# Performance work log

Hardware: AMD Instinct MI355X
Metric: run time of the kernel (lower is better)

The kernel has to match this reference:

```python
import math
import jax, jax.numpy as jnp
import numpy as np

D = 768      # hidden_size
H = 16       # num_attention_heads (hardcoded in module)
DH = D // H  # value dim per head
SEQ = 512    # fpos/tpos are taken modulo 512
EPS = 1e-5   # torch LayerNorm default
SCALE = math.sqrt(D / H)  # attention_head_size = dim_key_query_all / num_heads


def _collab_attn(h, fpos, tpos, Wq, Wk, Wcb, Wv, bv, mix, Wd, bd, lng, lnb):
    """CollaborativeAttention.forward on one segment. h: [SEQ, D]."""
    fpos = fpos % SEQ
    tpos = tpos % SEQ
    fs = h[fpos]                                   # [F, D] gathered 'from' nodes
    ts = h[tpos]                                   # [T, D] gathered 'to' nodes
    q = fs @ Wq.T                                  # [F, D] (no bias)
    k = ts @ Wk.T                                  # [T, D] (no bias)
    mq = q[None, :, :] * mix[:, None, :]           # [H, F, D] per-head mixing
    scores = jnp.einsum('hfd,td->hft', mq, k)      # [H, F, T] full-D contraction
    cb = (ts @ Wcb.T).T                            # [H, T] content bias
    scores = (scores + cb[:, None, :]) / SCALE
    probs = jax.nn.softmax(scores, axis=-1)        # dropout = identity at eval
    v = (ts @ Wv.T + bv).reshape(-1, H, DH).transpose(1, 0, 2)  # [H, T, DH]
    ctx = jnp.einsum('hft,htd->hfd', probs, v)     # [H, F, DH]
    ctx = ctx.transpose(1, 0, 2).reshape(-1, D) @ Wd.T + bd      # [F, D]
    x = fs + ctx                                   # residual on gathered nodes
    mu = x.mean(-1, keepdims=True)
    var = ((x - mu) ** 2).mean(-1, keepdims=True)
    return lng * (x - mu) / jnp.sqrt(var + EPS) + lnb


def _encoder(hidden_states, fpos, tpos, qtoc, ctoq):
    outs = []
    for b in range(3):  # fixed small segment count, matches original unrolling
        o1 = _collab_attn(hidden_states[b], fpos[b], tpos[b], *qtoc).mean(0)
        o2 = _collab_attn(hidden_states[b], tpos[b], fpos[b], *ctoq).mean(0)
        outs.append(jnp.concatenate([o1, o2]))
    return jnp.stack(outs)  # [3, 2*D]


def setup_inputs() -> dict:
    key = jax.random.key(0)
    ks = jax.random.split(key, 32)
    inp = {
        'hidden_states': jax.random.normal(ks[0], (3, SEQ, D), jnp.float32),
        'fpos': jax.random.randint(ks[1], (3, 2048), 0, SEQ, jnp.int32),
        'tpos': jax.random.randint(ks[2], (3, 2048), 0, SEQ, jnp.int32),
    }
    i = 3
    for p in ('qtoc', 'ctoq'):
        for n, shape, std in (('Wq', (D, D), 0.02), ('Wk', (D, D), 0.02),
                              ('Wcb', (H, D), 0.02), ('Wv', (D, D), 0.02),
                              ('Wd', (D, D), 0.02), ('mix', (H, D), 0.2)):
            inp[p + '_' + n] = std * jax.random.normal(ks[i], shape, jnp.float32)
            i += 1
        inp[p + '_bv'] = jnp.zeros((D,), jnp.float32)
        inp[p + '_bd'] = jnp.zeros((D,), jnp.float32)
        inp[p + '_lng'] = jnp.ones((D,), jnp.float32)
        inp[p + '_lnb'] = jnp.zeros((D,), jnp.float32)
    return inp


def reference(hidden_states, fpos, tpos,
              qtoc_Wq, qtoc_Wk, qtoc_Wcb, qtoc_Wv, qtoc_Wd, qtoc_mix,
              qtoc_bv, qtoc_bd, qtoc_lng, qtoc_lnb,
              ctoq_Wq, ctoq_Wk, ctoq_Wcb, ctoq_Wv, ctoq_Wd, ctoq_mix,
              ctoq_bv, ctoq_bd, ctoq_lng, ctoq_lnb):
    qtoc = (qtoc_Wq, qtoc_Wk, qtoc_Wcb, qtoc_Wv, qtoc_bv, qtoc_mix,
            qtoc_Wd, qtoc_bd, qtoc_lng, qtoc_lnb)
    ctoq = (ctoq_Wq, ctoq_Wk, ctoq_Wcb, ctoq_Wv, ctoq_bv, ctoq_mix,
            ctoq_Wd, ctoq_bd, ctoq_lng, ctoq_lnb)
    return _encoder(hidden_states, fpos, tpos, qtoc, ctoq)
```

## Files before the change

kernel.cpp:

```cpp
#include <hip/hip_runtime.h>
#include <math.h>

#define DD 768
#define HH 16
#define DHH 48
#define NPOS 512
#define NIDX 2048
#define INV_SCALE 0.14433756729740643f
#define LN_EPS 1e-5f

typedef __bf16 bf16_t;
typedef __bf16 bf16x8 __attribute__((ext_vector_type(8)));
typedef float f32x4 __attribute__((ext_vector_type(4)));

__device__ __forceinline__ void g2lds16(const void* g, void* l) {
  __builtin_amdgcn_global_load_lds((const __attribute__((address_space(1))) void*)g,
                                   (__attribute__((address_space(3))) void*)l, 16, 0, 0);
}
__device__ __forceinline__ int stg_chunk(int lane) { return (lane & 3) ^ ((lane >> 3) & 3); }
__device__ __forceinline__ int rd_off(int row, int lq) {
  return row * 32 + ((lq ^ ((row >> 1) & 3)) << 3);
}

struct CvtDesc { const float* src; bf16_t* dst; int n8; };
struct CvtBatch { CvtDesc d[13]; };

__global__ __launch_bounds__(256) void prep(const int* __restrict__ fpos,
                                            const int* __restrict__ tpos,
                                            int* __restrict__ CNT, CvtBatch cvb) {
  const int bid = blockIdx.x;
  const int tid = threadIdx.x;
  __shared__ int shist[NPOS];
  if (bid < 6) {
    const int b = bid >> 1, which = bid & 1;
    const int* src = (which ? tpos : fpos) + b * NIDX;
    for (int i = tid; i < NPOS; i += 256) shist[i] = 0;
    __syncthreads();
    for (int i = tid; i < NIDX; i += 256) atomicAdd(&shist[src[i] & (NPOS - 1)], 1);
    __syncthreads();
    for (int i = tid; i < NPOS; i += 256) CNT[bid * NPOS + i] = shist[i];
    return;
  }
  const CvtDesc de = cvb.d[(bid - 6) >> 6];
  for (int i = ((bid - 6) & 63) * 256 + tid; i < de.n8; i += 64 * 256) {
    bf16_t t[8];
    if (de.src) {
      const f32x4 a = *(const f32x4*)(de.src + (size_t)i * 8);
      const f32x4 b = *(const f32x4*)(de.src + (size_t)i * 8 + 4);
#pragma unroll
      for (int e = 0; e < 4; ++e) { t[e] = (bf16_t)a[e]; t[4 + e] = (bf16_t)b[e]; }
    } else {
#pragma unroll
      for (int e = 0; e < 8; ++e) t[e] = (bf16_t)0.f;
    }
    *(bf16x8*)(de.dst + (size_t)i * 8) = *(bf16x8*)t;
  }
}

struct MDesc { const bf16_t* A; const bf16_t* B; const float* bias; void* C;
               float* cb; int mode; int ntiles; };
struct MBatch { MDesc d[18]; };

__global__ __launch_bounds__(256, 4) void gemm64(MBatch batch) {
  const MDesc de = batch.d[blockIdx.y];
  const int mt = blockIdx.x & 7, nt = blockIdx.x >> 3;
  if (nt >= de.ntiles) return;
  const int m0 = mt * 64, n0 = nt * 128;

  __shared__ bf16_t SA[2][2048];
  __shared__ bf16_t SB[2][4096];

  const int tid = threadIdx.x;
  const int w = tid >> 6, lane = tid & 63;
  const int wm = w >> 1, wn = w & 1;
  const int lm = lane & 15, lq = lane >> 4;
  const int sr = lane >> 2, sc = stg_chunk(lane);

  f32x4 acc[2][4] = {};

  auto stage = [&](int buf, int k0) {
#pragma unroll
    for (int c = 0; c < 3; ++c) {
      const int issue = w + c * 4;
      if (issue < 4)
        g2lds16(de.A + (size_t)(m0 + issue * 16 + sr) * 768 + k0 + sc * 8,
                SA[buf] + issue * 512);
      else {
        const int e = issue - 4;
        g2lds16(de.B + (size_t)(n0 + e * 16 + sr) * 768 + k0 + sc * 8,
                SB[buf] + e * 512);
      }
    }
  };

  stage(0, 0);
  for (int k0i = 0; k0i < 24; ++k0i) {
    const int cur = k0i & 1;
    __syncthreads();
    if (k0i + 1 < 24) stage(cur ^ 1, (k0i + 1) * 32);
    bf16x8 af[2], bfr[4];
#pragma unroll
    for (int i = 0; i < 2; ++i)
      af[i] = *(const bf16x8*)(SA[cur] + rd_off(wm * 32 + i * 16 + lm, lq));
#pragma unroll
    for (int j = 0; j < 4; ++j)
      bfr[j] = *(const bf16x8*)(SB[cur] + rd_off(wn * 64 + j * 16 + lm, lq));
#pragma unroll
    for (int i = 0; i < 2; ++i)
#pragma unroll
      for (int j = 0; j < 4; ++j)
        acc[i][j] = __builtin_amdgcn_mfma_f32_16x16x32_bf16(af[i], bfr[j], acc[i][j], 0, 0, 0);
  }

#pragma unroll
  for (int i = 0; i < 2; ++i) {
    const int rbase = m0 + wm * 32 + i * 16 + lq * 4;
#pragma unroll
    for (int j = 0; j < 4; ++j) {
      const int c = n0 + wn * 64 + j * 16 + lm;
      const float bv = (de.bias && c < 768) ? de.bias[c] : 0.f;
#pragma unroll
      for (int r = 0; r < 4; ++r) {
        const float v = acc[i][j][r] + bv;
        if (de.mode == 0)      ((float*)de.C)[(size_t)(rbase + r) * 768 + c] = v;
        else if (de.mode == 1) ((bf16_t*)de.C)[(size_t)(rbase + r) * 768 + c] = (bf16_t)v;
        else if (de.mode == 2) ((bf16_t*)de.C)[(size_t)c * NPOS + rbase + r] = (bf16_t)v;
        else {
          if (c < 768)       ((bf16_t*)de.C)[(size_t)(rbase + r) * 768 + c] = (bf16_t)v;
          else if (c < 784)  de.cb[(size_t)(rbase + r) * 16 + (c - 768)] = v;
        }
      }
    }
  }
}

__global__ __launch_bounds__(512, 4) void attn_mfma(
    const bf16_t* __restrict__ Qg, const bf16_t* __restrict__ Kg,
    const bf16_t* __restrict__ Vt, const float* __restrict__ cbG,
    const int* __restrict__ CNT, const float* __restrict__ mix0,
    const float* __restrict__ mix1, bf16_t* __restrict__ CTX) {
  const int bid = blockIdx.x;
  const int pd = bid >> 7;
  const int hg = (bid >> 4) & 7;
  const int ft = bid & 15;
  const int dir = pd & 1;
  const int f0 = ft * 32;

  __shared__ bf16_t U[17408];
  __shared__ bf16_t Vs[64 * 264];
  __shared__ float mixs[2][768];
  __shared__ float cbw[2][512];
  __shared__ float rowl[2][32];

  const int tid = threadIdx.x;
  const int w = tid >> 6, lane = tid & 63;
  const int hh = w & 1, jq = w >> 1;
  const int lm = lane & 15, lq = lane >> 4;
  const int sr = lane >> 2, sc = stg_chunk(lane);

  const bf16_t* Qp = Qg + (size_t)pd * NPOS * DD;
  const bf16_t* Kp = Kg + (size_t)pd * NPOS * DD;
  const float* mixsel = dir ? mix1 : mix0;
  const int* cnt = CNT + ((pd & ~1) + (1 - dir)) * NPOS;

  for (int i = tid; i < 2 * 768; i += 512) {
    const int h2 = i / 768, c = i % 768;
    mixs[h2][c] = mixsel[(hg * 2 + h2) * DD + c] * INV_SCALE;
  }
  for (int i = tid; i < 2 * 512; i += 512) {
    const int h2 = i >> 9, j = i & 511;
    cbw[h2][j] = cbG[((size_t)pd * NPOS + j) * HH + hg * 2 + h2] * INV_SCALE
               + __logf((float)cnt[j]);
  }
  for (int i = tid; i < 16 * 264; i += 512) {
    const int r = 48 + i / 264, c = i % 264;
    Vs[r * 264 + c] = (bf16_t)((r == 48 && c < 256) ? 1.f : 0.f);
  }

  f32x4 sa[2][8] = {};

  for (int k0i = 0; k0i < 24; ++k0i) {
    const int k0 = k0i * 32;
    __syncthreads();
#pragma unroll
    for (int c = 0; c < 5; ++c) {
      const int issue = w + c * 8;
      if (issue < 2)
        g2lds16(Qp + (size_t)(f0 + issue * 16 + sr) * DD + k0 + sc * 8,
                U + issue * 512);
      else if (issue < 34) {
        const int e = issue - 2;
        g2lds16(Kp + (size_t)(e * 16 + sr) * DD + k0 + sc * 8,
                U + 1024 + e * 512);
      }
    }
    __syncthreads();

    const f32x4 mxa = *(const f32x4*)&mixs[hh][k0 + lq * 8];
    const f32x4 mxb = *(const f32x4*)&mixs[hh][k0 + lq * 8 + 4];
    bf16x8 af[2];
#pragma unroll
    for (int i = 0; i < 2; ++i) {
      const bf16x8 q = *(const bf16x8*)(U + rd_off(i * 16 + lm, lq));
      bf16_t t[8];
#pragma unroll
      for (int e = 0; e < 4; ++e) {
        t[e]     = (bf16_t)((float)q[e] * mxa[e]);
        t[4 + e] = (bf16_t)((float)q[4 + e] * mxb[e]);
      }
      af[i] = *(bf16x8*)t;
    }
#pragma unroll
    for (int jj = 0; jj < 8; ++jj) {
      const bf16x8 bf = *(const bf16x8*)(U + 1024 + rd_off(jq * 128 + jj * 16 + lm, lq));
      sa[0][jj] = __builtin_amdgcn_mfma_f32_16x16x32_bf16(af[0], bf, sa[0][jj], 0, 0, 0);
      sa[1][jj] = __builtin_amdgcn_mfma_f32_16x16x32_bf16(af[1], bf, sa[1][jj], 0, 0, 0);
    }
  }
  __syncthreads();

  const int fi = w & 1, cj = w >> 1;
  f32x4 pv[2] = {};

  for (int ph = 0; ph < 2; ++ph) {
    const int h = hg * 2 + ph;
    const bf16_t* Vp = Vt + (size_t)pd * DD * NPOS + (size_t)h * DHH * NPOS;

    if (hh == ph) {
#pragma unroll
      for (int jj = 0; jj < 8; ++jj) {
        const int col = jq * 128 + jj * 16 + lm;
        const float cb = cbw[ph][col];
#pragma unroll
        for (int i = 0; i < 2; ++i) {
          const int rb = i * 16 + lq * 4;
#pragma unroll
          for (int r = 0; r < 4; ++r)
            U[(rb + r) * 532 + col] = (bf16_t)__expf(sa[i][jj][r] + cb);
        }
      }
    }

    for (int vh = 0; vh < 2; ++vh) {
      for (int i = tid; i < 48 * 32; i += 512) {
        const int r = i >> 5, cc = i & 31;
        *(bf16x8*)(Vs + r * 264 + cc * 8) =
            *(const bf16x8*)(Vp + (size_t)r * NPOS + vh * 256 + cc * 8);
      }
      __syncthreads();
#pragma unroll
      for (int kk = 0; kk < 8; ++kk) {
        const bf16x8 pa = *(const bf16x8*)(U + (fi * 16 + lm) * 532 + vh * 256 + kk * 32 + lq * 8);
        const bf16x8 pb = *(const bf16x8*)(Vs + (cj * 16 + lm) * 264 + kk * 32 + lq * 8);
        pv[ph] = __builtin_amdgcn_mfma_f32_16x16x32_bf16(pa, pb, pv[ph], 0, 0, 0);
      }
      __syncthreads();
    }
    if (cj == 3 && lm == 0) {
#pragma unroll
      for (int r = 0; r < 4; ++r) rowl[ph][fi * 16 + lq * 4 + r] = pv[ph][r];
    }
  }
  __syncthreads();

  if (cj < 3) {
#pragma unroll
    for (int ph = 0; ph < 2; ++ph) {
      const int h = hg * 2 + ph;
#pragma unroll
      for (int r = 0; r < 4; ++r) {
        const int fr = fi * 16 + lq * 4 + r;
        CTX[((size_t)pd * NPOS + f0 + fr) * DD + h * DHH + cj * 16 + lm] =
            (bf16_t)(pv[ph][r] / rowl[ph][fr]);
      }
    }
  }
}

__global__ __launch_bounds__(256) void ln_mean_kernel(
    const float* __restrict__ hs, const float* __restrict__ XB,
    const int* __restrict__ CNT,
    const float* __restrict__ lng0, const float* __restrict__ lnb0,
    const float* __restrict__ lng1, const float* __restrict__ lnb1,
    float* __restrict__ out) {
  const int blk = blockIdx.x;
  const int chunk = blk & 63;
  const int pd = blk >> 6;
  const int b = pd >> 1, dir = pd & 1;
  const float* lng = dir ? lng1 : lng0;
  const float* lnb = dir ? lnb1 : lnb0;
  const int* cnt = CNT + pd * NPOS;
  const float* hb = hs + (size_t)b * NPOS * DD;
  const float* xb = XB + (size_t)pd * NPOS * DD;

  __shared__ float wacc[4][DD];
  const int tid = threadIdx.x;
  const int wave = tid >> 6, lane = tid & 63;
  for (int d0 = tid; d0 < 4 * DD; d0 += 256) ((float*)wacc)[d0] = 0.f;
  __syncthreads();

  float lg[12], lb[12];
#pragma unroll
  for (int qd = 0; qd < 12; ++qd) {
    lg[qd] = lng[lane + qd * 64];
    lb[qd] = lnb[lane + qd * 64];
  }

  for (int rr = 0; rr < 2; ++rr) {
    const int p = chunk * 8 + wave * 2 + rr;
    float x[12];
    float s = 0.f, ss = 0.f;
#pragma unroll
    for (int qd = 0; qd < 12; ++qd) {
      const int d0 = lane + qd * 64;
      const float xv = hb[(size_t)p * DD + d0] + xb[(size_t)p * DD + d0];
      x[qd] = xv; s += xv; ss += xv * xv;
    }
#pragma unroll
    for (int o = 1; o < 64; o <<= 1) {
      s += __shfl_xor(s, o);
      ss += __shfl_xor(ss, o);
    }
    const float mu = s * (1.f / 768.f);
    const float var = ss * (1.f / 768.f) - mu * mu;
    const float rstd = rsqrtf(var + LN_EPS);
    const float wgt = (float)cnt[p];
    if (wgt != 0.f) {
#pragma unroll
      for (int qd = 0; qd < 12; ++qd) {
        const int d0 = lane + qd * 64;
        wacc[wave][d0] += wgt * (lg[qd] * (x[qd] - mu) * rstd + lb[qd]);
      }
    }
  }
  __syncthreads();
  for (int d0 = tid; d0 < DD; d0 += 256) {
    const float t = wacc[0][d0] + wacc[1][d0] + wacc[2][d0] + wacc[3][d0];
    atomicAdd(&out[b * 1536 + dir * 768 + d0], t * (1.f / 2048.f));
  }
}

extern "C" void kernel_launch(void* const* d_in, const int* in_sizes, int n_in,
                              void* d_out, int out_size, void* d_ws, size_t ws_size,
                              hipStream_t stream) {
  const float* hs  = (const float*)d_in[0];
  const int* fpos  = (const int*)d_in[1];
  const int* tpos  = (const int*)d_in[2];

  const float* Wq[2]; const float* Wk[2]; const float* Wcb[2]; const float* Wv[2];
  const float* Wd[2]; const float* mixp[2];
  const float* bv[2]; const float* bd[2]; const float* lng[2]; const float* lnb[2];
  for (int p = 0; p < 2; ++p) {
    const int base = 3 + p * 10;
    Wq[p]   = (const float*)d_in[base + 0];
    Wk[p]   = (const float*)d_in[base + 1];
    Wcb[p]  = (const float*)d_in[base + 2];
    Wv[p]   = (const float*)d_in[base + 3];
    Wd[p]   = (const float*)d_in[base + 4];
    mixp[p] = (const float*)d_in[base + 5];
    bv[p]   = (const float*)d_in[base + 6];
    bd[p]   = (const float*)d_in[base + 7];
    lng[p]  = (const float*)d_in[base + 8];
    lnb[p]  = (const float*)d_in[base + 9];
  }

  char* wsp = (char*)d_ws;
  size_t off = 0;
  auto alloc = [&](size_t bytes) { char* p = wsp + off; off = (off + bytes + 255) & ~(size_t)255; return p; };
  bf16_t* hsb  = (bf16_t*)alloc((size_t)3 * NPOS * DD * 2);
  bf16_t* Wb   = (bf16_t*)alloc((size_t)6 * DD * DD * 2);
  bf16_t* WkCb = (bf16_t*)alloc((size_t)2 * 896 * DD * 2);
  bf16_t* Qbf  = (bf16_t*)alloc((size_t)6 * NPOS * DD * 2);
  bf16_t* Kbf  = (bf16_t*)alloc((size_t)6 * NPOS * DD * 2);
  bf16_t* VtG  = (bf16_t*)alloc((size_t)6 * DD * NPOS * 2);
  bf16_t* CTXb = (bf16_t*)alloc((size_t)6 * NPOS * DD * 2);
  float*  XB   = (float*) alloc((size_t)6 * NPOS * DD * 4);
  float*  cbG  = (float*) alloc((size_t)6 * NPOS * HH * 4);
  int*    CNTb = (int*)   alloc((size_t)6 * NPOS * 4);

  hipMemsetAsync(d_out, 0, (size_t)out_size * sizeof(float), stream);

  CvtBatch cvb{};
  cvb.d[0] = CvtDesc{hs, hsb, 3 * NPOS * DD / 8};
  for (int p = 0; p < 2; ++p) {
    cvb.d[1 + p * 3] = CvtDesc{Wq[p], Wb + (size_t)(p * 3 + 0) * DD * DD, DD * DD / 8};
    cvb.d[2 + p * 3] = CvtDesc{Wv[p], Wb + (size_t)(p * 3 + 1) * DD * DD, DD * DD / 8};
    cvb.d[3 + p * 3] = CvtDesc{Wd[p], Wb + (size_t)(p * 3 + 2) * DD * DD, DD * DD / 8};
    bf16_t* wk = WkCb + (size_t)p * 896 * DD;
    cvb.d[7 + p * 3] = CvtDesc{Wk[p], wk, DD * DD / 8};
    cvb.d[8 + p * 3] = CvtDesc{Wcb[p], wk + (size_t)768 * DD, 16 * DD / 8};
    cvb.d[9 + p * 3] = CvtDesc{nullptr, wk + (size_t)784 * DD, 112 * DD / 8};
  }
  prep<<<838, 256, 0, stream>>>(fpos, tpos, CNTb, cvb);

  MBatch gb{};
  int n = 0;
  for (int b = 0; b < 3; ++b)
    for (int p = 0; p < 2; ++p) {
      const int pd = b * 2 + p;
      const bf16_t* A = hsb + (size_t)b * NPOS * DD;
      const size_t o = (size_t)pd * NPOS * DD;
      gb.d[n++] = MDesc{A, Wb + (size_t)(p * 3 + 0) * DD * DD, nullptr, Qbf + o, nullptr, 1, 6};
      gb.d[n++] = MDesc{A, WkCb + (size_t)p * 896 * DD, nullptr, Kbf + o,
                        cbG + (size_t)pd * NPOS * HH, 3, 7};
      gb.d[n++] = MDesc{A, Wb + (size_t)(p * 3 + 1) * DD * DD, bv[p],
                        VtG + (size_t)pd * DD * NPOS, nullptr, 2, 6};
    }
  gemm64<<<dim3(56, 18), 256, 0, stream>>>(gb);

  attn_mfma<<<768, 512, 0, stream>>>(Qbf, Kbf, VtG, cbG, CNTb, mixp[0], mixp[1], CTXb);

  MBatch gd{};
  for (int b = 0; b < 3; ++b)
    for (int p = 0; p < 2; ++p) {
      const int pd = b * 2 + p;
      const size_t o = (size_t)pd * NPOS * DD;
      gd.d[pd] = MDesc{CTXb + o, Wb + (size_t)(p * 3 + 2) * DD * DD, bd[p],
                       XB + o, nullptr, 0, 6};
    }
  gemm64<<<dim3(56, 6), 256, 0, stream>>>(gd);

  ln_mean_kernel<<<384, 256, 0, stream>>>(hs, XB, CNTb, lng[0], lnb[0], lng[1], lnb[1],
                                          (float*)d_out);
}
```

Before: 250.0 us.

## Register-prefetch K/Q and V tiles to overlap global loads with MFMA

Replaces the direct global-to-LDS async loads for the Q/K score loop with a register double-buffer. The next k-slice is loaded into registers while MFMAs run on the current slice, then written to LDS after the barrier. The PV phase gets the same treatment: the next V tile is prefetched into registers, which removes one barrier per step and folds the exp/prob write into the first sub-step. This adds register pressure and swaps the LDS-direct loads for register round-trips, so it may lower occupancy.

```diff
diff --git a/kernel.cpp b/kernel.cpp
--- a/kernel.cpp
+++ b/kernel.cpp
@@ -177,24 +177,36 @@
     Vs[r * 264 + c] = (bf16_t)((r == 48 && c < 256) ? 1.f : 0.f);
   }
 
+  bf16x8 kreg[4];
+  bf16x8 qreg;
+  auto load_stage = [&](int k0) {
+#pragma unroll
+    for (int c = 0; c < 4; ++c) {
+      const int e = w * 4 + c;
+      kreg[c] = *(const bf16x8*)(Kp + (size_t)(e * 16 + sr) * DD + k0 + sc * 8);
+    }
+    if (w < 2)
+      qreg = *(const bf16x8*)(Qp + (size_t)(f0 + w * 16 + sr) * DD + k0 + sc * 8);
+  };
+  auto write_stage = [&]() {
+#pragma unroll
+    for (int c = 0; c < 4; ++c) {
+      const int e = w * 4 + c;
+      *(bf16x8*)(U + 1024 + e * 512 + lane * 8) = kreg[c];
+    }
+    if (w < 2)
+      *(bf16x8*)(U + w * 512 + lane * 8) = qreg;
+  };
+
   f32x4 sa[2][8] = {};
 
+  load_stage(0);
   for (int k0i = 0; k0i < 24; ++k0i) {
     const int k0 = k0i * 32;
     __syncthreads();
-#pragma unroll
-    for (int c = 0; c < 5; ++c) {
-      const int issue = w + c * 8;
-      if (issue < 2)
-        g2lds16(Qp + (size_t)(f0 + issue * 16 + sr) * DD + k0 + sc * 8,
-                U + issue * 512);
-      else if (issue < 34) {
-        const int e = issue - 2;
-        g2lds16(Kp + (size_t)(e * 16 + sr) * DD + k0 + sc * 8,
-                U + 1024 + e * 512);
-      }
-    }
+    write_stage();
     __syncthreads();
+    if (k0i + 1 < 24) load_stage(k0 + 32);
 
     const f32x4 mxa = *(const f32x4*)&mixs[hh][k0 + lq * 8];
     const f32x4 mxb = *(const f32x4*)&mixs[hh][k0 + lq * 8 + 4];
@@ -217,44 +229,58 @@
       sa[1][jj] = __builtin_amdgcn_mfma_f32_16x16x32_bf16(af[1], bf, sa[1][jj], 0, 0, 0);
     }
   }
-  __syncthreads();
 
   const int fi = w & 1, cj = w >> 1;
+  const bf16_t* Vp0 = Vt + (size_t)pd * DD * NPOS + (size_t)(hg * 2) * DHH * NPOS;
+  const bf16_t* Vp1 = Vp0 + (size_t)DHH * NPOS;
+
+  bf16x8 vreg[3];
+  auto load_vs = [&](const bf16_t* Vp, int vh) {
+#pragma unroll
+    for (int u = 0; u < 3; ++u) {
+      const int s = tid + u * 512, r = s >> 5, cc = s & 31;
+      vreg[u] = *(const bf16x8*)(Vp + (size_t)r * NPOS + vh * 256 + cc * 8);
+    }
+  };
+  auto write_vs = [&]() {
+#pragma unroll
+    for (int u = 0; u < 3; ++u) {
+      const int s = tid + u * 512, r = s >> 5, cc = s & 31;
+      *(bf16x8*)(Vs + r * 264 + cc * 8) = vreg[u];
+    }
+  };
+
+  load_vs(Vp0, 0);
   f32x4 pv[2] = {};
 
   for (int ph = 0; ph < 2; ++ph) {
-    const int h = hg * 2 + ph;
-    const bf16_t* Vp = Vt + (size_t)pd * DD * NPOS + (size_t)h * DHH * NPOS;
-
-    if (hh == ph) {
-#pragma unroll
-      for (int jj = 0; jj < 8; ++jj) {
-        const int col = jq * 128 + jj * 16 + lm;
-        const float cb = cbw[ph][col];
-#pragma unroll
-        for (int i = 0; i < 2; ++i) {
-          const int rb = i * 16 + lq * 4;
-#pragma unroll
-          for (int r = 0; r < 4; ++r)
-            U[(rb + r) * 532 + col] = (bf16_t)__expf(sa[i][jj][r] + cb);
+    for (int vh = 0; vh < 2; ++vh) {
+      __syncthreads();
+      write_vs();
+      if (hh == ph && vh == 0) {
+#pragma unroll
+        for (int jj = 0; jj < 8; ++jj) {
+          const int col = jq * 128 + jj * 16 + lm;
+          const float cb = cbw[ph][col];
+#pragma unroll
+          for (int i = 0; i < 2; ++i) {
+            const int rb = i * 16 + lq * 4;
+#pragma unroll
+            for (int r = 0; r < 4; ++r)
+              U[(rb + r) * 532 + col] = (bf16_t)__expf(sa[i][jj][r] + cb);
+          }
         }
       }
-    }
-
-    for (int vh = 0; vh < 2; ++vh) {
-      for (int i = tid; i < 48 * 32; i += 512) {
-        const int r = i >> 5, cc = i & 31;
-        *(bf16x8*)(Vs + r * 264 + cc * 8) =
-            *(const bf16x8*)(Vp + (size_t)r * NPOS + vh * 256 + cc * 8);
-      }
       __syncthreads();
+      if (ph == 0 && vh == 0)      load_vs(Vp0, 1);
+      else if (ph == 0 && vh == 1) load_vs(Vp1, 0);
+      else if (ph == 1 && vh == 0) load_vs(Vp1, 1);
 #pragma unroll
       for (int kk = 0; kk < 8; ++kk) {
         const bf16x8 pa = *(const bf16x8*)(U + (fi * 16 + lm) * 532 + vh * 256 + kk * 32 + lq * 8);
         const bf16x8 pb = *(const bf16x8*)(Vs + (cj * 16 + lm) * 264 + kk * 32 + lq * 8);
         pv[ph] = __builtin_amdgcn_mfma_f32_16x16x32_bf16(pa, pb, pv[ph], 0, 0, 0);
       }
-      __syncthreads();
     }
     if (cj == 3 && lm == 0) {
 #pragma unroll
```

Result: faster. 236.1 us (-5.6%).

## Retile attention kernel to one head per block with register-prefetched K and V

Applied to the files above, without the earlier changes.

The attention kernel now gives each block one head and 64 'from' rows instead of two heads and 32 rows. K fragments are loaded straight from global memory into registers and double-buffered, rather than staged through LDS with global_load_lds. Mixed Q is written once per k-step into a small LDS tile, and the V tiles are prefetched into registers while the previous tile is consumed. The aim is to overlap global loads with MFMA work and raise per-block reuse of K across more query rows. In exchange, K is loaded by every block without LDS sharing, and register pressure rises.

```diff
diff --git a/kernel.cpp b/kernel.cpp
--- a/kernel.cpp
+++ b/kernel.cpp
@@ -140,138 +140,145 @@
     const int* __restrict__ CNT, const float* __restrict__ mix0,
     const float* __restrict__ mix1, bf16_t* __restrict__ CTX) {
   const int bid = blockIdx.x;
-  const int pd = bid >> 7;
-  const int hg = (bid >> 4) & 7;
-  const int ft = bid & 15;
+  const int ft = bid & 7, h = (bid >> 3) & 15, pd = bid >> 7;
   const int dir = pd & 1;
-  const int f0 = ft * 32;
-
-  __shared__ bf16_t U[17408];
-  __shared__ bf16_t Vs[64 * 264];
-  __shared__ float mixs[2][768];
-  __shared__ float cbw[2][512];
+  const int f0 = ft * 64;
+
+  __shared__ bf16_t QM[2048];
+  __shared__ bf16_t P[32 * 532];
+  __shared__ bf16_t Vs[64 * 268];
+  __shared__ float mixs[768];
+  __shared__ float cbw[512];
   __shared__ float rowl[2][32];
 
   const int tid = threadIdx.x;
   const int w = tid >> 6, lane = tid & 63;
-  const int hh = w & 1, jq = w >> 1;
   const int lm = lane & 15, lq = lane >> 4;
-  const int sr = lane >> 2, sc = stg_chunk(lane);
 
   const bf16_t* Qp = Qg + (size_t)pd * NPOS * DD;
   const bf16_t* Kp = Kg + (size_t)pd * NPOS * DD;
-  const float* mixsel = dir ? mix1 : mix0;
+  const bf16_t* Vp = Vt + (size_t)pd * DD * NPOS + (size_t)h * DHH * NPOS;
+  const float* mixsel = (dir ? mix1 : mix0) + h * DD;
   const int* cnt = CNT + ((pd & ~1) + (1 - dir)) * NPOS;
 
-  for (int i = tid; i < 2 * 768; i += 512) {
-    const int h2 = i / 768, c = i % 768;
-    mixs[h2][c] = mixsel[(hg * 2 + h2) * DD + c] * INV_SCALE;
-  }
-  for (int i = tid; i < 2 * 512; i += 512) {
-    const int h2 = i >> 9, j = i & 511;
-    cbw[h2][j] = cbG[((size_t)pd * NPOS + j) * HH + hg * 2 + h2] * INV_SCALE
-               + __logf((float)cnt[j]);
-  }
-  for (int i = tid; i < 16 * 264; i += 512) {
-    const int r = 48 + i / 264, c = i % 264;
-    Vs[r * 264 + c] = (bf16_t)((r == 48 && c < 256) ? 1.f : 0.f);
-  }
-
-  f32x4 sa[2][8] = {};
-
+  for (int i = tid; i < 768; i += 512) mixs[i] = mixsel[i] * INV_SCALE;
+  if (tid < 512)
+    cbw[tid] = cbG[((size_t)pd * NPOS + tid) * HH + h] * INV_SCALE
+             + __logf((float)cnt[tid]);
+  for (int i = tid; i < 268; i += 512)
+    Vs[48 * 268 + i] = (bf16_t)((i < 256) ? 1.f : 0.f);
+
+  const int qr = (tid & 255) >> 2, qp = tid & 3;
+  const int qg = qp ^ ((qr >> 1) & 3);
+  const bf16_t* qsrc = Qp + (size_t)(f0 + qr) * DD + qg * 8;
+
+  const bf16_t* ksrc = Kp + (size_t)(w * 64 + lm) * DD + lq * 8;
+
+  f32x4 sa[4][4] = {};
+  bf16x8 breg[2][4];
+  bf16x8 qreg[2];
+
+#pragma unroll
+  for (int jj = 0; jj < 4; ++jj)
+    breg[0][jj] = *(const bf16x8*)(ksrc + (size_t)jj * 16 * DD);
+  if (tid < 256) qreg[0] = *(const bf16x8*)qsrc;
+
+#pragma unroll
   for (int k0i = 0; k0i < 24; ++k0i) {
+    const int cur = k0i & 1;
     const int k0 = k0i * 32;
     __syncthreads();
-#pragma unroll
-    for (int c = 0; c < 5; ++c) {
-      const int issue = w + c * 8;
-      if (issue < 2)
-        g2lds16(Qp + (size_t)(f0 + issue * 16 + sr) * DD + k0 + sc * 8,
-                U + issue * 512);
-      else if (issue < 34) {
-        const int e = issue - 2;
-        g2lds16(Kp + (size_t)(e * 16 + sr) * DD + k0 + sc * 8,
-                U + 1024 + e * 512);
-      }
+    if (tid < 256) {
+      const f32x4 m0v = *(const f32x4*)&mixs[k0 + qg * 8];
+      const f32x4 m1v = *(const f32x4*)&mixs[k0 + qg * 8 + 4];
+      const bf16x8 q = qreg[cur];
+      bf16_t t[8];
+#pragma unroll
+      for (int e = 0; e < 4; ++e) {
+        t[e]     = (bf16_t)((float)q[e] * m0v[e]);
+        t[4 + e] = (bf16_t)((float)q[4 + e] * m1v[e]);
+      }
+      *(bf16x8*)(QM + qr * 32 + qp * 8) = *(bf16x8*)t;
     }
     __syncthreads();
-
-    const f32x4 mxa = *(const f32x4*)&mixs[hh][k0 + lq * 8];
-    const f32x4 mxb = *(const f32x4*)&mixs[hh][k0 + lq * 8 + 4];
-    bf16x8 af[2];
-#pragma unroll
-    for (int i = 0; i < 2; ++i) {
-      const bf16x8 q = *(const bf16x8*)(U + rd_off(i * 16 + lm, lq));
-      bf16_t t[8];
-#pragma unroll
-      for (int e = 0; e < 4; ++e) {
-        t[e]     = (bf16_t)((float)q[e] * mxa[e]);
-        t[4 + e] = (bf16_t)((float)q[4 + e] * mxb[e]);
-      }
-      af[i] = *(bf16x8*)t;
-    }
-#pragma unroll
-    for (int jj = 0; jj < 8; ++jj) {
-      const bf16x8 bf = *(const bf16x8*)(U + 1024 + rd_off(jq * 128 + jj * 16 + lm, lq));
-      sa[0][jj] = __builtin_amdgcn_mfma_f32_16x16x32_bf16(af[0], bf, sa[0][jj], 0, 0, 0);
-      sa[1][jj] = __builtin_amdgcn_mfma_f32_16x16x32_bf16(af[1], bf, sa[1][jj], 0, 0, 0);
+    if (k0i + 1 < 24) {
+#pragma unroll
+      for (int jj = 0; jj < 4; ++jj)
+        breg[cur ^ 1][jj] = *(const bf16x8*)(ksrc + (size_t)jj * 16 * DD + k0 + 32);
+      if (tid < 256) qreg[cur ^ 1] = *(const bf16x8*)(qsrc + k0 + 32);
+    }
+#pragma unroll
+    for (int i = 0; i < 4; ++i) {
+      const bf16x8 af = *(const bf16x8*)(QM + rd_off(i * 16 + lm, lq));
+#pragma unroll
+      for (int jj = 0; jj < 4; ++jj)
+        sa[i][jj] = __builtin_amdgcn_mfma_f32_16x16x32_bf16(af, breg[cur][jj], sa[i][jj], 0, 0, 0);
+    }
+  }
+
+  const int fi = w & 1, cj = w >> 1;
+  bf16x8 vreg[3];
+  auto load_vs = [&](int vh) {
+#pragma unroll
+    for (int u = 0; u < 3; ++u) {
+      const int s = tid + u * 512, r = s >> 5, cc = s & 31;
+      vreg[u] = *(const bf16x8*)(Vp + (size_t)r * NPOS + vh * 256 + cc * 8);
+    }
+  };
+  auto write_vs = [&]() {
+#pragma unroll
+    for (int u = 0; u < 3; ++u) {
+      const int s = tid + u * 512, r = s >> 5, cc = s & 31;
+      *(bf16x8*)(Vs + r * 268 + cc * 8) = vreg[u];
+    }
+  };
+
+  load_vs(0);
+  f32x4 pv[2] = {};
+
+  for (int fh = 0; fh < 2; ++fh) {
+    for (int vh = 0; vh < 2; ++vh) {
+      __syncthreads();
+      write_vs();
+      if (vh == 0) {
+#pragma unroll
+        for (int il = 0; il < 2; ++il) {
+#pragma unroll
+          for (int jj = 0; jj < 4; ++jj) {
+            const int col = w * 64 + jj * 16 + lm;
+            const float cb = cbw[col];
+#pragma unroll
+            for (int r = 0; r < 4; ++r)
+              P[(il * 16 + lq * 4 + r) * 532 + col] =
+                  (bf16_t)__expf(sa[fh * 2 + il][jj][r] + cb);
+          }
+        }
+      }
+      __syncthreads();
+      if (fh == 0)      load_vs(vh ^ 1);
+      else if (vh == 0) load_vs(1);
+#pragma unroll
+      for (int kk = 0; kk < 8; ++kk) {
+        const bf16x8 pa = *(const bf16x8*)(P + (fi * 16 + lm) * 532 + vh * 256 + kk * 32 + lq * 8);
+        const bf16x8 pb = *(const bf16x8*)(Vs + (cj * 16 + lm) * 268 + kk * 32 + lq * 8);
+        pv[fh] = __builtin_amdgcn_mfma_f32_16x16x32_bf16(pa, pb, pv[fh], 0, 0, 0);
+      }
+    }
+    if (cj == 3 && lm == 0) {
+#pragma unroll
+      for (int r = 0; r < 4; ++r) rowl[fh][fi * 16 + lq * 4 + r] = pv[fh][r];
     }
   }
   __syncthreads();
 
-  const int fi = w & 1, cj = w >> 1;
-  f32x4 pv[2] = {};
-
-  for (int ph = 0; ph < 2; ++ph) {
-    const int h = hg * 2 + ph;
-    const bf16_t* Vp = Vt + (size_t)pd * DD * NPOS + (size_t)h * DHH * NPOS;
-
-    if (hh == ph) {
-#pragma unroll
-      for (int jj = 0; jj < 8; ++jj) {
-        const int col = jq * 128 + jj * 16 + lm;
-        const float cb = cbw[ph][col];
-#pragma unroll
-        for (int i = 0; i < 2; ++i) {
-          const int rb = i * 16 + lq * 4;
-#pragma unroll
-          for (int r = 0; r < 4; ++r)
-            U[(rb + r) * 532 + col] = (bf16_t)__expf(sa[i][jj][r] + cb);
-        }
-      }
-    }
-
-    for (int vh = 0; vh < 2; ++vh) {
-      for (int i = tid; i < 48 * 32; i += 512) {
-        const int r = i >> 5, cc = i & 31;
-        *(bf16x8*)(Vs + r * 264 + cc * 8) =
-            *(const bf16x8*)(Vp + (size_t)r * NPOS + vh * 256 + cc * 8);
-      }
-      __syncthreads();
-#pragma unroll
-      for (int kk = 0; kk < 8; ++kk) {
-        const bf16x8 pa = *(const bf16x8*)(U + (fi * 16 + lm) * 532 + vh * 256 + kk * 32 + lq * 8);
-        const bf16x8 pb = *(const bf16x8*)(Vs + (cj * 16 + lm) * 264 + kk * 32 + lq * 8);
-        pv[ph] = __builtin_amdgcn_mfma_f32_16x16x32_bf16(pa, pb, pv[ph], 0, 0, 0);
-      }
-      __syncthreads();
-    }
-    if (cj == 3 && lm == 0) {
-#pragma unroll
-      for (int r = 0; r < 4; ++r) rowl[ph][fi * 16 + lq * 4 + r] = pv[ph][r];
-    }
-  }
-  __syncthreads();
-
   if (cj < 3) {
 #pragma unroll
-    for (int ph = 0; ph < 2; ++ph) {
-      const int h = hg * 2 + ph;
+    for (int fh = 0; fh < 2; ++fh) {
 #pragma unroll
       for (int r = 0; r < 4; ++r) {
         const int fr = fi * 16 + lq * 4 + r;
-        CTX[((size_t)pd * NPOS + f0 + fr) * DD + h * DHH + cj * 16 + lm] =
-            (bf16_t)(pv[ph][r] / rowl[ph][fr]);
+        CTX[((size_t)pd * NPOS + f0 + fh * 32 + fr) * DD + h * DHH + cj * 16 + lm] =
+            (bf16_t)(pv[fh][r] / rowl[fh][fr]);
       }
     }
   }
```

Result: slower. 263.5 us (+5.4%).
